# Kernel tuning notes

Measured on AMD Instinct MI355X. Metric: run time of the kernel, lower is better.

## Reference

```python
import jax, jax.numpy as jnp
import numpy as np

D_MODEL = 1024
HIDDEN = 4096
NUM_EXPERTS = 8
NUM_GROUPS = 4      # from _compute_group_size(4, 4096) with max_group_size=4096
GROUP_SIZE = 4096
EXPERT_CAPACITY = 512  # round(1.0 * 4096 / 8), >= max(8, 4096//100)


def setup_inputs() -> dict:
    key = jax.random.key(0)
    ks = jax.random.split(key, 10)
    s_in = 1.0 / np.sqrt(D_MODEL)
    s_hid = 1.0 / np.sqrt(HIDDEN)
    return {
        "x": jax.random.normal(ks[0], (4, 4096, D_MODEL), dtype=jnp.float32),
        "gate_w": jax.random.normal(ks[1], (D_MODEL, NUM_EXPERTS), dtype=jnp.float32) * 0.1,
        "gate_b": jax.random.normal(ks[2], (NUM_EXPERTS,), dtype=jnp.float32) * 0.01,
        "temperature": jnp.ones((1,), dtype=jnp.float32),
        "shared_w1": jax.random.normal(ks[3], (D_MODEL, HIDDEN), dtype=jnp.float32) * s_in,
        "shared_b1": jnp.zeros((HIDDEN,), dtype=jnp.float32),
        "shared_w2": jax.random.normal(ks[4], (HIDDEN, D_MODEL), dtype=jnp.float32) * s_hid,
        "shared_b2": jnp.zeros((D_MODEL,), dtype=jnp.float32),
        "expert_w1": jax.random.normal(ks[5], (NUM_EXPERTS, D_MODEL, HIDDEN), dtype=jnp.float32) * s_in,
        "expert_b1": jnp.zeros((NUM_EXPERTS, HIDDEN), dtype=jnp.float32),
        "expert_w2": jax.random.normal(ks[6], (NUM_EXPERTS, HIDDEN, D_MODEL), dtype=jnp.float32) * s_hid,
        "expert_b2": jnp.zeros((NUM_EXPERTS, D_MODEL), dtype=jnp.float32),
    }


def reference(x, gate_w, gate_b, temperature, shared_w1, shared_b1, shared_w2,
              shared_b2, expert_w1, expert_b1, expert_w2, expert_b2):
    B, S, D = x.shape
    T = NUM_GROUPS * GROUP_SIZE  # total tokens (no padding here)
    xg = x.reshape(NUM_GROUPS, GROUP_SIZE, D)

    # Router: softmax over temperature-scaled gate logits
    logits = jnp.einsum('gsd,de->gse', xg, gate_w) + gate_b
    safe_temp = jnp.maximum(temperature, 0.1)
    probs = jax.nn.softmax(logits / safe_temp, axis=-1)  # [G, Gs, E]
    # per-expert top-k over ALL tokens (flattened across groups)
    flat_probs = probs.transpose(2, 0, 1).reshape(NUM_EXPERTS, T)
    scores, tok_idx = jax.lax.top_k(flat_probs, EXPERT_CAPACITY)  # [E, C]

    # Shared expert FFN (gelu is tanh-approx, matching flax nn.gelu default)
    shared = jnp.einsum('gsh,hd->gsd',
                        jax.nn.gelu(jnp.einsum('gsd,dh->gsh', xg, shared_w1) + shared_b1),
                        shared_w2) + shared_b2

    # Routed experts: gather tokens, grouped FFN, weighted scatter-add
    x_flat = xg.reshape(T, D)
    tokens = x_flat[tok_idx]  # [E, C, D]
    h = jax.nn.gelu(jnp.einsum('ecd,edh->ech', tokens, expert_w1) + expert_b1[:, None, :])
    out_e = jnp.einsum('ech,ehd->ecd', h, expert_w2) + expert_b2[:, None, :]
    out_e = out_e * scores[..., None]
    routed = jnp.zeros_like(x_flat).at[tok_idx.reshape(-1)].add(out_e.reshape(-1, D))

    out = shared.reshape(T, D) + routed
    return out.reshape(B, S, D)
```

## Files before the change

### kernel.cpp

```cpp
#include <hip/hip_runtime.h>

#define NTOK 16384
#define DMODEL 1024
#define DHID 4096
#define NEXP 8
#define CAP 512

typedef __attribute__((ext_vector_type(8))) short bfrag_t;
typedef __attribute__((ext_vector_type(4))) float ffrag_t;

__device__ __forceinline__ unsigned short f2bf(float f) {
  unsigned u = __float_as_uint(f);
  u += 0x7FFFu + ((u >> 16) & 1u);
  return (unsigned short)(u >> 16);
}

__device__ __forceinline__ float gelu_fast(float x) {
  float t = x * x;
  float z = x * fmaf(0.071354814f, t, 1.5957691f);
  float e = __expf(-z);
  return x * __builtin_amdgcn_rcpf(1.0f + e);
}

__global__ void k_convert_bf16(const float* __restrict__ in, unsigned short* __restrict__ out, int n4) {
  int i = blockIdx.x * blockDim.x + threadIdx.x;
  int stride = gridDim.x * blockDim.x;
  for (; i < n4; i += stride) {
    float4 v = ((const float4*)in)[i];
    ushort4 o;
    o.x = f2bf(v.x); o.y = f2bf(v.y); o.z = f2bf(v.z); o.w = f2bf(v.w);
    ((ushort4*)out)[i] = o;
  }
}

__global__ void k_trans_conv(const float* __restrict__ in, unsigned short* __restrict__ out, int K, int N) {
  const size_t zb = blockIdx.z;
  in  += zb * (size_t)K * N;
  out += zb * (size_t)N * K;
  __shared__ float tile[32][33];
  const int n0 = blockIdx.x * 32, k0 = blockIdx.y * 32;
  const int tx = threadIdx.x & 31, ty = threadIdx.x >> 5;
#pragma unroll
  for (int i = 0; i < 4; ++i) {
    int k = ty + i * 8;
    tile[k][tx] = in[(size_t)(k0 + k) * N + n0 + tx];
  }
  __syncthreads();
#pragma unroll
  for (int i = 0; i < 4; ++i) {
    int n = ty + i * 8;
    out[(size_t)(n0 + n) * K + k0 + tx] = f2bf(tile[tx][n]);
  }
}

__global__ __launch_bounds__(256) void k_router(const float* __restrict__ x, const float* __restrict__ gw,
                                                const float* __restrict__ gb, const float* __restrict__ temp,
                                                float* __restrict__ probs) {
  __shared__ float gws[DMODEL * NEXP];
  for (int i = threadIdx.x; i < DMODEL * NEXP; i += 256) gws[i] = gw[i];
  __syncthreads();
  const int wave = threadIdx.x >> 6, lane = threadIdx.x & 63;
  const int t = blockIdx.x * 4 + wave;
  const float* xr = x + (size_t)t * DMODEL;
  float acc[NEXP];
#pragma unroll
  for (int e = 0; e < NEXP; ++e) acc[e] = 0.f;
  for (int d = lane; d < DMODEL; d += 64) {
    float xv = xr[d];
#pragma unroll
    for (int e = 0; e < NEXP; ++e) acc[e] += xv * gws[d * NEXP + e];
  }
#pragma unroll
  for (int off = 32; off >= 1; off >>= 1) {
#pragma unroll
    for (int e = 0; e < NEXP; ++e) acc[e] += __shfl_xor(acc[e], off);
  }
  if (lane == 0) {
    float st = fmaxf(temp[0], 0.1f);
    float m = -1e30f;
#pragma unroll
    for (int e = 0; e < NEXP; ++e) { acc[e] = (acc[e] + gb[e]) / st; m = fmaxf(m, acc[e]); }
    float s = 0.f;
#pragma unroll
    for (int e = 0; e < NEXP; ++e) { acc[e] = expf(acc[e] - m); s += acc[e]; }
    float inv = 1.f / s;
#pragma unroll
    for (int e = 0; e < NEXP; ++e) probs[(size_t)e * NTOK + t] = acc[e] * inv;
  }
}

__global__ __launch_bounds__(256) void k_topk(const float* __restrict__ probs, int* __restrict__ tok,
                                              float* __restrict__ scores, int* __restrict__ eqbuf) {
  const int e = blockIdx.x;
  const float* p = probs + (size_t)e * NTOK;
  int* eq = eqbuf + (size_t)e * NTOK;
  __shared__ int hist[256];
  __shared__ unsigned sh_pref;
  __shared__ int sh_k, sh_gt, sh_eq, sh_cnt;
  const int tid = threadIdx.x;
  if (tid == 0) { sh_pref = 0u; sh_k = CAP; }
  __syncthreads();
  for (int pass = 3; pass >= 0; --pass) {
    hist[tid] = 0;
    __syncthreads();
    const unsigned pref = sh_pref;
    const int shift = pass * 8;
    for (int t = tid; t < NTOK; t += 256) {
      unsigned key = __float_as_uint(p[t]);
      bool cand = (pass == 3) || ((key >> (shift + 8)) == pref);
      if (cand) atomicAdd(&hist[(key >> shift) & 255], 1);
    }
    __syncthreads();
    if (tid == 0) {
      int k = sh_k;
      int d = 255;
      while (hist[d] < k) { k -= hist[d]; --d; }
      sh_k = k;
      sh_pref = (pref << 8) | (unsigned)d;
    }
    __syncthreads();
  }
  const unsigned Kstar = sh_pref;
  const int need_eq = sh_k;
  if (tid == 0) { sh_gt = 0; sh_eq = 0; }
  __syncthreads();
  for (int t = tid; t < NTOK; t += 256) {
    unsigned key = __float_as_uint(p[t]);
    if (key > Kstar) {
      int pos = atomicAdd(&sh_gt, 1);
      tok[e * CAP + pos] = t;
      scores[e * CAP + pos] = p[t];
    } else if (key == Kstar) {
      int q = atomicAdd(&sh_eq, 1);
      eq[q] = t;
    }
  }
  __syncthreads();
  const int cg = sh_gt, ce = sh_eq;
  if (ce <= need_eq) {
    for (int j = tid; j < ce; j += 256) {
      tok[e * CAP + cg + j] = eq[j];
      scores[e * CAP + cg + j] = p[eq[j]];
    }
  } else {
    int lo = 0, hi = NTOK - 1;
    while (lo < hi) {
      int mid = (lo + hi) >> 1;
      if (tid == 0) sh_cnt = 0;
      __syncthreads();
      for (int j = tid; j < ce; j += 256)
        if (eq[j] <= mid) atomicAdd(&sh_cnt, 1);
      __syncthreads();
      if (sh_cnt >= need_eq) hi = mid; else lo = mid + 1;
      __syncthreads();
    }
    if (tid == 0) sh_cnt = 0;
    __syncthreads();
    for (int j = tid; j < ce; j += 256) {
      if (eq[j] <= lo) {
        int pos = cg + atomicAdd(&sh_cnt, 1);
        tok[e * CAP + pos] = eq[j];
        scores[e * CAP + pos] = p[eq[j]];
      }
    }
  }
}

__global__ void k_gather(const unsigned short* __restrict__ xb, const int* __restrict__ tok,
                         unsigned short* __restrict__ atok) {
  const int row = blockIdx.x;
  const int t = tok[row];
  const uint2* src = (const uint2*)(xb + (size_t)t * DMODEL);
  uint2* dst = (uint2*)(atok + (size_t)row * DMODEL);
  dst[threadIdx.x] = src[threadIdx.x];
}

template <int MODE>
__global__ __launch_bounds__(256, 4) void k_gemm(
    const unsigned short* __restrict__ A, const unsigned short* __restrict__ Bt,
    const float* __restrict__ bias, float* __restrict__ outF, unsigned short* __restrict__ outB,
    const int* __restrict__ tok, const float* __restrict__ scale,
    int M, int N, int Kloop, int LDK, int ksplit) {
  const int zb = blockIdx.z / ksplit;
  const int kc = blockIdx.z % ksplit;
  A += (size_t)zb * M * LDK + (size_t)kc * Kloop;
  Bt += (size_t)zb * N * LDK + (size_t)kc * Kloop;
  const float* bz = bias + (size_t)zb * N;

  const int gx = gridDim.x, gy = gridDim.y;
  const int nwg = gx * gy;
  const int id = blockIdx.x + blockIdx.y * gx;
  int bx, by;
  if ((gx & 7) == 0) {
    const int x = id & 7, c = id >> 3, H = gx >> 3;
    bx = x * H + (c % H);
    by = c / H;
  } else if ((nwg & 7) == 0) {
    const int q = nwg >> 3;
    const int sw = (id & 7) * q + (id >> 3);
    bx = sw % gx;
    by = sw / gx;
  } else {
    bx = blockIdx.x;
    by = blockIdx.y;
  }
  const int m0 = bx * 128, n0 = by * 128;

  const int tid = threadIdx.x, wave = tid >> 6, lane = tid & 63;
  const int wm = (wave >> 1) * 64, wn = (wave & 1) * 64;

  __shared__ alignas(16) unsigned short sh[128 * 128];
  unsigned short* As = sh;
  unsigned short* Bs = sh + 128 * 64;

  ffrag_t acc[4][4];
#pragma unroll
  for (int i = 0; i < 4; ++i)
#pragma unroll
    for (int j = 0; j < 4; ++j)
#pragma unroll
      for (int r = 0; r < 4; ++r) acc[i][j][r] = 0.f;

  int rr[4], gg[4], lb[4];
#pragma unroll
  for (int it = 0; it < 4; ++it) {
    int L = it * 256 + tid;
    rr[it] = L >> 3;
    gg[it] = (L & 7) ^ (rr[it] & 7);
    lb[it] = (it * 256 + wave * 64) * 16;
  }

  for (int kt = 0; kt < Kloop; kt += 64) {
#pragma unroll
    for (int it = 0; it < 4; ++it) {
      const unsigned short* sA = A + (size_t)(m0 + rr[it]) * LDK + kt + gg[it] * 8;
      const unsigned short* sB = Bt + (size_t)(n0 + rr[it]) * LDK + kt + gg[it] * 8;
      __builtin_amdgcn_global_load_lds((const __attribute__((address_space(1))) unsigned int*)sA,
                                       (__attribute__((address_space(3))) unsigned int*)((char*)As + lb[it]),
                                       16, 0, 0);
      __builtin_amdgcn_global_load_lds((const __attribute__((address_space(1))) unsigned int*)sB,
                                       (__attribute__((address_space(3))) unsigned int*)((char*)Bs + lb[it]),
                                       16, 0, 0);
    }
    __syncthreads();
#pragma unroll
    for (int kk = 0; kk < 2; ++kk) {
      bfrag_t af[4], bf[4];
      const int gl = kk * 4 + (lane >> 4);
#pragma unroll
      for (int mi = 0; mi < 4; ++mi) {
        int r = wm + mi * 16 + (lane & 15);
        af[mi] = *(const bfrag_t*)&As[r * 64 + ((gl ^ (r & 7)) * 8)];
      }
#pragma unroll
      for (int ni = 0; ni < 4; ++ni) {
        int r = wn + ni * 16 + (lane & 15);
        bf[ni] = *(const bfrag_t*)&Bs[r * 64 + ((gl ^ (r & 7)) * 8)];
      }
#pragma unroll
      for (int mi = 0; mi < 4; ++mi)
#pragma unroll
        for (int ni = 0; ni < 4; ++ni)
          acc[mi][ni] = __builtin_amdgcn_mfma_f32_16x16x32_bf16(af[mi], bf[ni], acc[mi][ni], 0, 0, 0);
    }
    __syncthreads();
  }

  const int rsub = (lane >> 4) * 4, cs = lane & 15;
  if (MODE == 0) {
    float bv[4];
#pragma unroll
    for (int ni = 0; ni < 4; ++ni) bv[ni] = bz[n0 + wn + ni * 16 + cs];
#pragma unroll
    for (int mi = 0; mi < 4; ++mi)
#pragma unroll
      for (int ni = 0; ni < 4; ++ni)
#pragma unroll
        for (int r = 0; r < 4; ++r) {
          float v = acc[mi][ni][r] + bv[ni];
          sh[(wm + mi * 16 + rsub + r) * 128 + (wn + ni * 16 + cs)] = f2bf(gelu_fast(v));
        }
    __syncthreads();
    const int seg = tid & 15, rw = tid >> 4;
#pragma unroll
    for (int rep = 0; rep < 8; ++rep) {
      const int row = rep * 16 + rw;
      uint4 v = *(const uint4*)&sh[row * 128 + seg * 8];
      *(uint4*)&outB[((size_t)zb * M + m0 + row) * N + n0 + seg * 8] = v;
    }
  } else if (MODE == 1) {
#pragma unroll
    for (int ni = 0; ni < 4; ++ni) {
      const int n = n0 + wn + ni * 16 + cs;
      const float bv = bz[n];
#pragma unroll
      for (int mi = 0; mi < 4; ++mi)
#pragma unroll
        for (int r = 0; r < 4; ++r) {
          const int m = m0 + wm + mi * 16 + rsub + r;
          outF[(size_t)m * N + n] = acc[mi][ni][r] + bv;
        }
    }
  } else {
#pragma unroll
    for (int ni = 0; ni < 4; ++ni) {
      const int n = n0 + wn + ni * 16 + cs;
      const float bv = (kc == 0) ? bz[n] : 0.f;
#pragma unroll
      for (int mi = 0; mi < 4; ++mi)
#pragma unroll
        for (int r = 0; r < 4; ++r) {
          const int m = m0 + wm + mi * 16 + rsub + r;
          const int t = tok[zb * M + m];
          const float s = scale[zb * M + m];
          atomicAdd(&outF[(size_t)t * N + n], (acc[mi][ni][r] + bv) * s);
        }
    }
  }
}

extern "C" void kernel_launch(void* const* d_in, const int* in_sizes, int n_in,
                              void* d_out, int out_size, void* d_ws, size_t ws_size,
                              hipStream_t stream) {
  const float* x      = (const float*)d_in[0];
  const float* gate_w = (const float*)d_in[1];
  const float* gate_b = (const float*)d_in[2];
  const float* temp   = (const float*)d_in[3];
  const float* sw1    = (const float*)d_in[4];
  const float* sb1    = (const float*)d_in[5];
  const float* sw2    = (const float*)d_in[6];
  const float* sb2    = (const float*)d_in[7];
  const float* ew1    = (const float*)d_in[8];
  const float* eb1    = (const float*)d_in[9];
  const float* ew2    = (const float*)d_in[10];
  const float* eb2    = (const float*)d_in[11];
  float* out = (float*)d_out;

  char* ws = (char*)d_ws;
  size_t o = 0;
  auto take = [&](size_t bytes) { char* p = ws + o; o += (bytes + 255) & ~(size_t)255; return p; };
  unsigned short* x_bf = (unsigned short*)take((size_t)NTOK * DMODEL * 2);
  unsigned short* w1t  = (unsigned short*)take((size_t)DMODEL * DHID * 2);
  unsigned short* w2t  = (unsigned short*)take((size_t)DHID * DMODEL * 2);
  unsigned short* ew1t = (unsigned short*)take((size_t)NEXP * DMODEL * DHID * 2);
  unsigned short* ew2t = (unsigned short*)take((size_t)NEXP * DHID * DMODEL * 2);
  float* probs         = (float*)take((size_t)NEXP * NTOK * 4);
  int* tok             = (int*)take((size_t)NEXP * CAP * 4);
  float* scores        = (float*)take((size_t)NEXP * CAP * 4);
  int* eqbuf           = (int*)take((size_t)NEXP * NTOK * 4);
  unsigned short* atok = (unsigned short*)take((size_t)NEXP * CAP * DMODEL * 2);
  unsigned short* he   = (unsigned short*)take((size_t)NEXP * CAP * DHID * 2);
  unsigned short* hs   = (unsigned short*)take((size_t)NTOK * DHID * 2);

  k_convert_bf16<<<4096, 256, 0, stream>>>(x, x_bf, NTOK * DMODEL / 4);
  k_trans_conv<<<dim3(DHID / 32, DMODEL / 32, 1), 256, 0, stream>>>(sw1, w1t, DMODEL, DHID);
  k_trans_conv<<<dim3(DMODEL / 32, DHID / 32, 1), 256, 0, stream>>>(sw2, w2t, DHID, DMODEL);
  k_trans_conv<<<dim3(DHID / 32, DMODEL / 32, NEXP), 256, 0, stream>>>(ew1, ew1t, DMODEL, DHID);
  k_trans_conv<<<dim3(DMODEL / 32, DHID / 32, NEXP), 256, 0, stream>>>(ew2, ew2t, DHID, DMODEL);

  k_router<<<NTOK / 4, 256, 0, stream>>>(x, gate_w, gate_b, temp, probs);
  k_topk<<<NEXP, 256, 0, stream>>>(probs, tok, scores, eqbuf);
  k_gather<<<NEXP * CAP, 256, 0, stream>>>(x_bf, tok, atok);

  k_gemm<0><<<dim3(128, 32, 1), 256, 0, stream>>>(
      x_bf, w1t, sb1, nullptr, hs, nullptr, nullptr, NTOK, DHID, DMODEL, DMODEL, 1);
  k_gemm<1><<<dim3(128, 8, 1), 256, 0, stream>>>(
      hs, w2t, sb2, out, nullptr, nullptr, nullptr, NTOK, DMODEL, DHID, DHID, 1);

  k_gemm<0><<<dim3(4, 32, NEXP), 256, 0, stream>>>(
      atok, ew1t, eb1, nullptr, he, nullptr, nullptr, CAP, DHID, DMODEL, DMODEL, 1);
  k_gemm<2><<<dim3(4, 8, NEXP * 4), 256, 0, stream>>>(
      he, ew2t, eb2, out, nullptr, tok, scores, CAP, DMODEL, DHID / 4, DHID, 4);
}
```

Measured before the change: 700.8 us.

## Add 256x256 double-buffered GEMM, fuse bf16 convert into router, gather in GEMM

The shared first FFN GEMM now uses a new 512-thread kernel with 256x256 tiles, double-buffered LDS staging, interleaved MFMA blocks and setprio hints. The standalone x-to-bf16 conversion is folded into the router, and the expert token gather is folded into the expert GEMM's A-row addressing. The weight transpose now uses 64x64 tiles with 16-byte stores, and the remaining GEMM's launch bounds rise to 5 waves per SIMD. Together these aim to cut kernel launches, extra memory passes and the tile-load overhead of the largest GEMM. The trade-off is heavier register and LDS use in the new kernel and a more serialised router.

```diff
diff --git a/kernel.cpp b/kernel.cpp
--- a/kernel.cpp
+++ b/kernel.cpp
@@ -22,51 +22,49 @@
   return x * __builtin_amdgcn_rcpf(1.0f + e);
 }
 
-__global__ void k_convert_bf16(const float* __restrict__ in, unsigned short* __restrict__ out, int n4) {
-  int i = blockIdx.x * blockDim.x + threadIdx.x;
-  int stride = gridDim.x * blockDim.x;
-  for (; i < n4; i += stride) {
-    float4 v = ((const float4*)in)[i];
-    ushort4 o;
-    o.x = f2bf(v.x); o.y = f2bf(v.y); o.z = f2bf(v.z); o.w = f2bf(v.w);
-    ((ushort4*)out)[i] = o;
-  }
-}
-
-__global__ void k_trans_conv(const float* __restrict__ in, unsigned short* __restrict__ out, int K, int N) {
+__global__ __launch_bounds__(256) void k_trans64(const float* __restrict__ in,
+                                                 unsigned short* __restrict__ out, int K, int N) {
   const size_t zb = blockIdx.z;
   in  += zb * (size_t)K * N;
   out += zb * (size_t)N * K;
-  __shared__ float tile[32][33];
-  const int n0 = blockIdx.x * 32, k0 = blockIdx.y * 32;
-  const int tx = threadIdx.x & 31, ty = threadIdx.x >> 5;
-#pragma unroll
-  for (int i = 0; i < 4; ++i) {
-    int k = ty + i * 8;
+  __shared__ float tile[64][65];
+  const int n0 = blockIdx.x * 64, k0 = blockIdx.y * 64;
+  const int tx = threadIdx.x & 63, ty = threadIdx.x >> 6;
+#pragma unroll
+  for (int i = 0; i < 16; ++i) {
+    const int k = ty * 16 + i;
     tile[k][tx] = in[(size_t)(k0 + k) * N + n0 + tx];
   }
   __syncthreads();
-#pragma unroll
-  for (int i = 0; i < 4; ++i) {
-    int n = ty + i * 8;
-    out[(size_t)(n0 + n) * K + k0 + tx] = f2bf(tile[tx][n]);
+  const int sx = threadIdx.x & 7, sy = threadIdx.x >> 3;
+#pragma unroll
+  for (int j = 0; j < 2; ++j) {
+    const int n = sy + j * 32;
+    uint4 v;
+    v.x = (unsigned)f2bf(tile[sx * 8 + 0][n]) | ((unsigned)f2bf(tile[sx * 8 + 1][n]) << 16);
+    v.y = (unsigned)f2bf(tile[sx * 8 + 2][n]) | ((unsigned)f2bf(tile[sx * 8 + 3][n]) << 16);
+    v.z = (unsigned)f2bf(tile[sx * 8 + 4][n]) | ((unsigned)f2bf(tile[sx * 8 + 5][n]) << 16);
+    v.w = (unsigned)f2bf(tile[sx * 8 + 6][n]) | ((unsigned)f2bf(tile[sx * 8 + 7][n]) << 16);
+    *(uint4*)&out[(size_t)(n0 + n) * K + k0 + sx * 8] = v;
   }
 }
 
 __global__ __launch_bounds__(256) void k_router(const float* __restrict__ x, const float* __restrict__ gw,
                                                 const float* __restrict__ gb, const float* __restrict__ temp,
-                                                float* __restrict__ probs) {
+                                                float* __restrict__ probs, unsigned short* __restrict__ xb) {
   __shared__ float gws[DMODEL * NEXP];
   for (int i = threadIdx.x; i < DMODEL * NEXP; i += 256) gws[i] = gw[i];
   __syncthreads();
   const int wave = threadIdx.x >> 6, lane = threadIdx.x & 63;
   const int t = blockIdx.x * 4 + wave;
   const float* xr = x + (size_t)t * DMODEL;
+  unsigned short* xw = xb + (size_t)t * DMODEL;
   float acc[NEXP];
 #pragma unroll
   for (int e = 0; e < NEXP; ++e) acc[e] = 0.f;
   for (int d = lane; d < DMODEL; d += 64) {
     float xv = xr[d];
+    xw[d] = f2bf(xv);
 #pragma unroll
     for (int e = 0; e < NEXP; ++e) acc[e] += xv * gws[d * NEXP + e];
   }
@@ -166,27 +164,44 @@
   }
 }
 
-__global__ void k_gather(const unsigned short* __restrict__ xb, const int* __restrict__ tok,
-                         unsigned short* __restrict__ atok) {
-  const int row = blockIdx.x;
-  const int t = tok[row];
-  const uint2* src = (const uint2*)(xb + (size_t)t * DMODEL);
-  uint2* dst = (uint2*)(atok + (size_t)row * DMODEL);
-  dst[threadIdx.x] = src[threadIdx.x];
-}
+#define WAITV2() asm volatile("s_waitcnt vmcnt(2)" ::: "memory")
+#define WAITV0() asm volatile("s_waitcnt vmcnt(0)" ::: "memory")
+#define BAR()                      \
+  do {                             \
+    asm volatile("" ::: "memory"); \
+    __builtin_amdgcn_s_barrier();  \
+    asm volatile("" ::: "memory"); \
+  } while (0)
+
+#define GL(SRC, DOFF)                                                          \
+  __builtin_amdgcn_global_load_lds(                                            \
+      (const __attribute__((address_space(1))) unsigned int*)(SRC),            \
+      (__attribute__((address_space(3))) unsigned int*)(lds + (DOFF)), 16, 0, 0)
+
+#define STG_A(J, T, NB) GL(gsA[J] + (size_t)(T) * 64, (NB) + (J) * 8192 + wave * 1024)
+#define STG_B(J, T, NB) GL(gsB[J] + (size_t)(T) * 64, (NB) + 32768 + (J) * 8192 + wave * 1024)
+
+#define RD_AF(X0, XK)                                                            \
+  _Pragma("unroll") for (int _i = 0; _i < 4; ++_i)                               \
+      af[_i] = *(const bfrag_t*)(base + (aoff[(X0) + _i] ^ (XK)))
+#define RD_BF(XK)                                                                \
+  _Pragma("unroll") for (int _n = 0; _n < 4; ++_n)                               \
+      bf[_n] = *(const bfrag_t*)(base + (boff[_n] ^ (XK)))
+
+#define MFMA16(MB)                                                                           \
+  __builtin_amdgcn_s_setprio(1);                                                             \
+  _Pragma("unroll") for (int _m = 0; _m < 4; ++_m) {                                         \
+    _Pragma("unroll") for (int _n = 0; _n < 4; ++_n)                                         \
+        acc[(MB) + _m][_n] = __builtin_amdgcn_mfma_f32_16x16x32_bf16(                        \
+            af[_m], bf[_n], acc[(MB) + _m][_n], 0, 0, 0);                                    \
+  }                                                                                          \
+  __builtin_amdgcn_s_setprio(0)
 
 template <int MODE>
-__global__ __launch_bounds__(256, 4) void k_gemm(
+__global__ __launch_bounds__(512, 2) void k_gemm8(
     const unsigned short* __restrict__ A, const unsigned short* __restrict__ Bt,
     const float* __restrict__ bias, float* __restrict__ outF, unsigned short* __restrict__ outB,
-    const int* __restrict__ tok, const float* __restrict__ scale,
-    int M, int N, int Kloop, int LDK, int ksplit) {
-  const int zb = blockIdx.z / ksplit;
-  const int kc = blockIdx.z % ksplit;
-  A += (size_t)zb * M * LDK + (size_t)kc * Kloop;
-  Bt += (size_t)zb * N * LDK + (size_t)kc * Kloop;
-  const float* bz = bias + (size_t)zb * N;
-
+    int M, int N, int K) {
   const int gx = gridDim.x, gy = gridDim.y;
   const int nwg = gx * gy;
   const int id = blockIdx.x + blockIdx.y * gx;
@@ -204,6 +219,172 @@
     bx = blockIdx.x;
     by = blockIdx.y;
   }
+  const int m0 = bx * 256, n0 = by * 256;
+
+  const int tid = threadIdx.x, wave = tid >> 6, lane = tid & 63;
+  const int wm = (wave >> 2) * 128;
+  const int wn = (wave & 3) * 64;
+
+  __shared__ alignas(16) char lds[131072];
+
+  ffrag_t acc[8][4];
+#pragma unroll
+  for (int i = 0; i < 8; ++i)
+#pragma unroll
+    for (int j = 0; j < 4; ++j)
+#pragma unroll
+      for (int r = 0; r < 4; ++r) acc[i][j][r] = 0.f;
+
+  const unsigned short* gsA[4];
+  const unsigned short* gsB[4];
+#pragma unroll
+  for (int j = 0; j < 4; ++j) {
+    const int L = j * 512 + tid;
+    const int row = L >> 3;
+    const int g = (L & 7) ^ (row & 7);
+    gsA[j] = A + (size_t)(m0 + row) * K + g * 8;
+    gsB[j] = Bt + (size_t)(n0 + row) * K + g * 8;
+  }
+
+  int aoff[8], boff[4];
+#pragma unroll
+  for (int mi = 0; mi < 8; ++mi) {
+    const int row = wm + mi * 16 + (lane & 15);
+    aoff[mi] = row * 128 + ((((lane >> 4)) ^ (row & 7)) << 4);
+  }
+#pragma unroll
+  for (int ni = 0; ni < 4; ++ni) {
+    const int row = wn + ni * 16 + (lane & 15);
+    boff[ni] = 32768 + row * 128 + ((((lane >> 4)) ^ (row & 7)) << 4);
+  }
+
+  const int NT = K >> 6;
+
+  STG_B(0, 0, 0); STG_B(1, 0, 0); STG_B(2, 0, 0); STG_B(3, 0, 0);
+  STG_A(0, 0, 0); STG_A(2, 0, 0); STG_A(1, 0, 0); STG_A(3, 0, 0);
+  WAITV2();
+  BAR();
+
+  bfrag_t af[4], bf[4];
+
+  for (int t = 0; t < NT - 1; ++t) {
+    const char* base = lds + ((t & 1) << 16);
+    const int nb = ((t + 1) & 1) << 16;
+    RD_AF(0, 0);
+    RD_BF(0);
+    STG_B(0, t + 1, nb); STG_B(1, t + 1, nb);
+    WAITV2();
+    BAR();
+    MFMA16(0);
+    BAR();
+    RD_AF(4, 0);
+    STG_B(2, t + 1, nb); STG_B(3, t + 1, nb);
+    BAR();
+    MFMA16(4);
+    BAR();
+    RD_AF(0, 64);
+    RD_BF(64);
+    STG_A(0, t + 1, nb); STG_A(2, t + 1, nb);
+    BAR();
+    MFMA16(0);
+    BAR();
+    RD_AF(4, 64);
+    STG_A(1, t + 1, nb); STG_A(3, t + 1, nb);
+    WAITV2();
+    BAR();
+    MFMA16(4);
+    BAR();
+  }
+  {
+    const char* base = lds + (((NT - 1) & 1) << 16);
+    RD_AF(0, 0);
+    RD_BF(0);
+    WAITV0();
+    BAR();
+    MFMA16(0);
+    BAR();
+    RD_AF(4, 0);
+    BAR();
+    MFMA16(4);
+    BAR();
+    RD_AF(0, 64);
+    RD_BF(64);
+    BAR();
+    MFMA16(0);
+    BAR();
+    RD_AF(4, 64);
+    BAR();
+    MFMA16(4);
+    BAR();
+  }
+
+  const int rq = lane >> 4, cs = lane & 15;
+  if (MODE == 0) {
+    float bv[4];
+#pragma unroll
+    for (int ni = 0; ni < 4; ++ni) bv[ni] = bias[n0 + wn + ni * 16 + cs];
+    unsigned short* wbase = (unsigned short*)(lds + wave * 2304);
+#pragma unroll
+    for (int mi = 0; mi < 8; ++mi) {
+#pragma unroll
+      for (int ni = 0; ni < 4; ++ni)
+#pragma unroll
+        for (int r = 0; r < 4; ++r) {
+          float v = acc[mi][ni][r] + bv[ni];
+          wbase[(rq * 4 + r) * 72 + ni * 16 + cs] = f2bf(gelu_fast(v));
+        }
+      const int rrow = lane >> 3, uu = lane & 7;
+      uint4 v0 = *(const uint4*)((const char*)wbase + rrow * 144 + uu * 16);
+      uint4 v1 = *(const uint4*)((const char*)wbase + (rrow + 8) * 144 + uu * 16);
+      *(uint4*)&outB[((size_t)m0 + wm + mi * 16 + rrow) * N + n0 + wn + uu * 8] = v0;
+      *(uint4*)&outB[((size_t)m0 + wm + mi * 16 + rrow + 8) * N + n0 + wn + uu * 8] = v1;
+    }
+  } else {
+#pragma unroll
+    for (int ni = 0; ni < 4; ++ni) {
+      const int n = n0 + wn + ni * 16 + cs;
+      const float bv = bias[n];
+#pragma unroll
+      for (int mi = 0; mi < 8; ++mi)
+#pragma unroll
+        for (int r = 0; r < 4; ++r) {
+          const int m = m0 + wm + mi * 16 + rq * 4 + r;
+          outF[(size_t)m * N + n] = acc[mi][ni][r] + bv;
+        }
+    }
+  }
+}
+
+template <int MODE, bool GATHER>
+__global__ __launch_bounds__(256, 5) void k_gemm(
+    const unsigned short* __restrict__ A, const unsigned short* __restrict__ Bt,
+    const float* __restrict__ bias, float* __restrict__ outF, unsigned short* __restrict__ outB,
+    const int* __restrict__ tok, const float* __restrict__ scale,
+    int M, int N, int Kloop, int LDK, int ksplit) {
+  const int zb = blockIdx.z / ksplit;
+  const int kc = blockIdx.z % ksplit;
+  if (!GATHER) A += (size_t)zb * M * LDK;
+  A += (size_t)kc * Kloop;
+  Bt += (size_t)zb * N * LDK + (size_t)kc * Kloop;
+  const float* bz = bias + (size_t)zb * N;
+
+  const int gx = gridDim.x, gy = gridDim.y;
+  const int nwg = gx * gy;
+  const int id = blockIdx.x + blockIdx.y * gx;
+  int bx, by;
+  if ((gx & 7) == 0) {
+    const int x = id & 7, c = id >> 3, H = gx >> 3;
+    bx = x * H + (c % H);
+    by = c / H;
+  } else if ((nwg & 7) == 0) {
+    const int q = nwg >> 3;
+    const int sw = (id & 7) * q + (id >> 3);
+    bx = sw % gx;
+    by = sw / gx;
+  } else {
+    bx = blockIdx.x;
+    by = blockIdx.y;
+  }
   const int m0 = bx * 128, n0 = by * 128;
 
   const int tid = threadIdx.x, wave = tid >> 6, lane = tid & 63;
@@ -221,26 +402,30 @@
 #pragma unroll
       for (int r = 0; r < 4; ++r) acc[i][j][r] = 0.f;
 
-  int rr[4], gg[4], lb[4];
+  int lb[4];
+  const unsigned short* rowA[4];
+  const unsigned short* rowB[4];
 #pragma unroll
   for (int it = 0; it < 4; ++it) {
     int L = it * 256 + tid;
-    rr[it] = L >> 3;
-    gg[it] = (L & 7) ^ (rr[it] & 7);
+    int rr = L >> 3;
+    int gg = (L & 7) ^ (rr & 7);
     lb[it] = (it * 256 + wave * 64) * 16;
+    const unsigned short* ab =
+        GATHER ? (A + (size_t)tok[zb * M + m0 + rr] * LDK) : (A + (size_t)(m0 + rr) * LDK);
+    rowA[it] = ab + gg * 8;
+    rowB[it] = Bt + (size_t)(n0 + rr) * LDK + gg * 8;
   }
 
   for (int kt = 0; kt < Kloop; kt += 64) {
 #pragma unroll
     for (int it = 0; it < 4; ++it) {
-      const unsigned short* sA = A + (size_t)(m0 + rr[it]) * LDK + kt + gg[it] * 8;
-      const unsigned short* sB = Bt + (size_t)(n0 + rr[it]) * LDK + kt + gg[it] * 8;
-      __builtin_amdgcn_global_load_lds((const __attribute__((address_space(1))) unsigned int*)sA,
-                                       (__attribute__((address_space(3))) unsigned int*)((char*)As + lb[it]),
-                                       16, 0, 0);
-      __builtin_amdgcn_global_load_lds((const __attribute__((address_space(1))) unsigned int*)sB,
-                                       (__attribute__((address_space(3))) unsigned int*)((char*)Bs + lb[it]),
-                                       16, 0, 0);
+      __builtin_amdgcn_global_load_lds(
+          (const __attribute__((address_space(1))) unsigned int*)(rowA[it] + kt),
+          (__attribute__((address_space(3))) unsigned int*)((char*)As + lb[it]), 16, 0, 0);
+      __builtin_amdgcn_global_load_lds(
+          (const __attribute__((address_space(1))) unsigned int*)(rowB[it] + kt),
+          (__attribute__((address_space(3))) unsigned int*)((char*)Bs + lb[it]), 16, 0, 0);
     }
     __syncthreads();
 #pragma unroll
@@ -348,27 +533,24 @@
   int* tok             = (int*)take((size_t)NEXP * CAP * 4);
   float* scores        = (float*)take((size_t)NEXP * CAP * 4);
   int* eqbuf           = (int*)take((size_t)NEXP * NTOK * 4);
-  unsigned short* atok = (unsigned short*)take((size_t)NEXP * CAP * DMODEL * 2);
   unsigned short* he   = (unsigned short*)take((size_t)NEXP * CAP * DHID * 2);
   unsigned short* hs   = (unsigned short*)take((size_t)NTOK * DHID * 2);
 
-  k_convert_bf16<<<4096, 256, 0, stream>>>(x, x_bf, NTOK * DMODEL / 4);
-  k_trans_conv<<<dim3(DHID / 32, DMODEL / 32, 1), 256, 0, stream>>>(sw1, w1t, DMODEL, DHID);
-  k_trans_conv<<<dim3(DMODEL / 32, DHID / 32, 1), 256, 0, stream>>>(sw2, w2t, DHID, DMODEL);
-  k_trans_conv<<<dim3(DHID / 32, DMODEL / 32, NEXP), 256, 0, stream>>>(ew1, ew1t, DMODEL, DHID);
-  k_trans_conv<<<dim3(DMODEL / 32, DHID / 32, NEXP), 256, 0, stream>>>(ew2, ew2t, DHID, DMODEL);
-
-  k_router<<<NTOK / 4, 256, 0, stream>>>(x, gate_w, gate_b, temp, probs);
+  k_trans64<<<dim3(DHID / 64, DMODEL / 64, 1), 256, 0, stream>>>(sw1, w1t, DMODEL, DHID);
+  k_trans64<<<dim3(DMODEL / 64, DHID / 64, 1), 256, 0, stream>>>(sw2, w2t, DHID, DMODEL);
+  k_trans64<<<dim3(DHID / 64, DMODEL / 64, NEXP), 256, 0, stream>>>(ew1, ew1t, DMODEL, DHID);
+  k_trans64<<<dim3(DMODEL / 64, DHID / 64, NEXP), 256, 0, stream>>>(ew2, ew2t, DHID, DMODEL);
+
+  k_router<<<NTOK / 4, 256, 0, stream>>>(x, gate_w, gate_b, temp, probs, x_bf);
   k_topk<<<NEXP, 256, 0, stream>>>(probs, tok, scores, eqbuf);
-  k_gather<<<NEXP * CAP, 256, 0, stream>>>(x_bf, tok, atok);
-
-  k_gemm<0><<<dim3(128, 32, 1), 256, 0, stream>>>(
-      x_bf, w1t, sb1, nullptr, hs, nullptr, nullptr, NTOK, DHID, DMODEL, DMODEL, 1);
-  k_gemm<1><<<dim3(128, 8, 1), 256, 0, stream>>>(
+
+  k_gemm8<0><<<dim3(NTOK / 256, DHID / 256, 1), 512, 0, stream>>>(
+      x_bf, w1t, sb1, nullptr, hs, NTOK, DHID, DMODEL);
+  k_gemm<1, false><<<dim3(128, 8, 1), 256, 0, stream>>>(
       hs, w2t, sb2, out, nullptr, nullptr, nullptr, NTOK, DMODEL, DHID, DHID, 1);
 
-  k_gemm<0><<<dim3(4, 32, NEXP), 256, 0, stream>>>(
-      atok, ew1t, eb1, nullptr, he, nullptr, nullptr, CAP, DHID, DMODEL, DMODEL, 1);
-  k_gemm<2><<<dim3(4, 8, NEXP * 4), 256, 0, stream>>>(
+  k_gemm<0, true><<<dim3(4, 32, NEXP), 256, 0, stream>>>(
+      x_bf, ew1t, eb1, nullptr, he, tok, nullptr, CAP, DHID, DMODEL, DMODEL, 1);
+  k_gemm<2, false><<<dim3(4, 8, NEXP * 4), 256, 0, stream>>>(
       he, ew2t, eb2, out, nullptr, tok, scores, CAP, DMODEL, DHID / 4, DHID, 4);
 }
```

New measurement: 1.173 ms. 1.67x slower.
